# Kernel optimization log

Measured on AMD Instinct MI355X. Metric: run time of the kernel, lower is better.

The kernel has to match this reference:

```python
import math
import jax, jax.numpy as jnp
import numpy as np

B, S, D, H = 4, 2048, 1024, 16
HD = D // H
SAMPLING_FACTOR = 5.0


def setup_inputs() -> dict:
    key = jax.random.key(0)
    ks = jax.random.split(key, 6)
    std = 1.0 / math.sqrt(D)
    inp = {
        "x": jax.random.normal(ks[0], (B, S, D), dtype=jnp.float32),
        "Wq": jax.random.normal(ks[1], (D, D), dtype=jnp.float32) * std,
        "bq": jnp.zeros((D,), dtype=jnp.float32),
        "Wk": jax.random.normal(ks[2], (D, D), dtype=jnp.float32) * std,
        "bk": jnp.zeros((D,), dtype=jnp.float32),
        "Wv": jax.random.normal(ks[3], (D, D), dtype=jnp.float32) * std,
        "bv": jnp.zeros((D,), dtype=jnp.float32),
        "Wo": jax.random.normal(ks[4], (D, D), dtype=jnp.float32) * std,
        "bo": jnp.zeros((D,), dtype=jnp.float32),
        "sample_idx": jax.random.randint(ks[5], (S,), 0, S, dtype=jnp.int32),
    }
    return inp


def reference(x, Wq, bq, Wk, bk, Wv, bv, Wo, bo, sample_idx):
    batch, seq_len, d_model = x.shape
    scale = math.sqrt(HD)
    # u = number of top (active) queries; U_part = seq_len here (sampling saturates)
    u = max(1, min(seq_len, int(SAMPLING_FACTOR * math.log(seq_len + 1))))

    def proj(W, b):
        # [B,S,D] -> [B,H,S,hd]
        return (x @ W + b).reshape(batch, seq_len, H, HD).transpose(0, 2, 1, 3)

    Q = proj(Wq, bq)
    K = proj(Wk, bk)
    V = proj(Wv, bv)

    # sparsity measure over sampled keys (with replacement)
    K_sample = K[:, :, sample_idx, :]                     # [B,H,U,hd]
    scores_sample = jnp.einsum("bhsd,bhud->bhsu", Q, K_sample) / scale
    M = scores_sample.max(axis=-1) - scores_sample.mean(axis=-1)  # [B,H,S]

    _, top_idx = jax.lax.top_k(M, u)                      # [B,H,u]

    Q_reduce = jnp.take_along_axis(Q, top_idx[..., None], axis=2)  # [B,H,u,hd]
    attn_scores = jnp.einsum("bhud,bhsd->bhus", Q_reduce, K) / scale
    attn_probs = jax.nn.softmax(attn_scores, axis=-1)
    context = jnp.einsum("bhus,bhsd->bhud", attn_probs, V)        # [B,H,u,hd]

    # fill lazy queries with mean of V, scatter active-query contexts
    V_mean = V.mean(axis=2, keepdims=True)                # [B,H,1,hd]
    out = jnp.broadcast_to(V_mean, (batch, H, seq_len, HD))
    b_idx = jnp.arange(batch)[:, None, None]
    h_idx = jnp.arange(H)[None, :, None]
    out = out.at[b_idx, h_idx, top_idx].set(context)      # [B,H,S,hd]

    out = out.transpose(0, 2, 1, 3).reshape(batch, seq_len, d_model)
    return out @ Wo + bo
```

## Files before the change

### kernel.cpp

```cpp
#include <hip/hip_runtime.h>
#include <math.h>
#include <stdint.h>
#include <stddef.h>

#define BB 4
#define SS 2048
#define DD 1024
#define HH 16
#define HD 64
#define UU 38
#define BH (BB*HH)
#define NROWS (BB*SS)
#define QSZ (BB*HH*SS*HD)
#define NSPLIT 16
#define SPLEN (SS/NSPLIT)
#define QPAD 40

typedef unsigned short ushortT;
typedef unsigned int u32;
typedef __attribute__((ext_vector_type(8))) short bf16x8;
typedef __attribute__((ext_vector_type(4))) float f32x4;

static __device__ __forceinline__ ushortT f2bf(float f) {
  union { float f; unsigned int u; } v; v.f = f;
  unsigned int r = v.u + 0x7fffu + ((v.u >> 16) & 1u);
  return (ushortT)(r >> 16);
}
static __device__ __forceinline__ float bf2f(ushortT h) {
  union { unsigned int u; float f; } v; v.u = ((unsigned int)h) << 16; return v.f;
}
static __device__ __forceinline__ void gld16(const void* g, void* l) {
  __builtin_amdgcn_global_load_lds((const __attribute__((address_space(1))) u32*)g,
                                   (__attribute__((address_space(3))) u32*)l, 16, 0, 0);
}

__global__ __launch_bounds__(256) void split_x(
    const float* __restrict__ x, ushortT* __restrict__ xh, ushortT* __restrict__ xl)
{
  size_t i = ((size_t)blockIdx.x * 256 + threadIdx.x) * 8;
  float4 v0 = *(const float4*)&x[i];
  float4 v1 = *(const float4*)&x[i + 4];
  float fv[8] = {v0.x, v0.y, v0.z, v0.w, v1.x, v1.y, v1.z, v1.w};
  bf16x8 hv, lv;
#pragma unroll
  for (int j = 0; j < 8; ++j) {
    ushortT h = f2bf(fv[j]);
    hv[j] = (short)h;
    lv[j] = (short)f2bf(fv[j] - bf2f(h));
  }
  *(bf16x8*)&xh[i] = hv;
  *(bf16x8*)&xl[i] = lv;
}

__global__ __launch_bounds__(256) void splitT_kernel(
    const float* __restrict__ Wq, const float* __restrict__ Wk, const float* __restrict__ Wv,
    ushortT* __restrict__ WqhT, ushortT* __restrict__ WqlT,
    ushortT* __restrict__ WkhT, ushortT* __restrict__ WklT,
    ushortT* __restrict__ WvhT, ushortT* __restrict__ WvlT)
{
  __shared__ float tile[64][65];
  const int z = blockIdx.z;
  const float* W = (z == 0) ? Wq : (z == 1) ? Wk : Wv;
  ushortT* WhT = (z == 0) ? WqhT : (z == 1) ? WkhT : WvhT;
  ushortT* WlT = (z == 0) ? WqlT : (z == 1) ? WklT : WvlT;
  const int t = threadIdx.x;
  const int bk = blockIdx.y * 64, bn = blockIdx.x * 64;
  const int rr = t >> 4, c4 = (t & 15) * 4;
#pragma unroll
  for (int p = 0; p < 4; ++p) {
    int row = rr + p * 16;
    float4 v = *(const float4*)&W[(size_t)(bk + row) * DD + bn + c4];
    tile[row][c4] = v.x; tile[row][c4+1] = v.y; tile[row][c4+2] = v.z; tile[row][c4+3] = v.w;
  }
  __syncthreads();
  const int n = t & 63, ks = (t >> 6) * 16;
  union { ushortT us[16]; uint4 q[2]; } hb, lb;
#pragma unroll
  for (int j = 0; j < 16; ++j) {
    float f = tile[ks + j][n];
    ushortT h = f2bf(f);
    hb.us[j] = h;
    lb.us[j] = f2bf(f - bf2f(h));
  }
  size_t o = ((size_t)(bn + n) * DD + (size_t)(bk + ks)) >> 3;
  ((uint4*)WhT)[o] = hb.q[0]; ((uint4*)WhT)[o + 1] = hb.q[1];
  ((uint4*)WlT)[o] = lb.q[0]; ((uint4*)WlT)[o + 1] = lb.q[1];
}

__global__ __launch_bounds__(256) void dedupe_kernel(
    const int* __restrict__ sidx, int* __restrict__ uidx, int* __restrict__ ucount)
{
  __shared__ unsigned bm[64];
  __shared__ int base[64];
  const int t = threadIdx.x;
  if (t < 64) bm[t] = 0;
  __syncthreads();
  for (int s = t; s < SS; s += 256) {
    int v = sidx[s];
    atomicOr(&bm[v >> 5], 1u << (v & 31));
  }
  __syncthreads();
  if (t < 64) {
    int c = __popc(bm[t]);
    int pre = c;
#pragma unroll
    for (int off = 1; off < 64; off <<= 1) {
      int o = __shfl_up(pre, off, 64);
      if (t >= off) pre += o;
    }
    base[t] = pre - c;
    if (t == 63) ucount[0] = pre;
  }
  __syncthreads();
  if (t < 64) {
    unsigned m = bm[t];
    int o = base[t];
    while (m) {
      int b = __ffs(m) - 1;
      uidx[o++] = t * 32 + b;
      m &= m - 1;
    }
  }
  __syncthreads();
  int total = ucount[0];
  int padded = (total + 127) & ~127;
  int first = uidx[0];
  for (int i = total + t; i < padded; i += 256) uidx[i] = first;
}

__global__ __launch_bounds__(256, 4) void gemm_qkv(
    const ushortT* __restrict__ Axh, const ushortT* __restrict__ Axl,
    const ushortT* __restrict__ WqhT, const ushortT* __restrict__ WqlT,
    const ushortT* __restrict__ WkhT, const ushortT* __restrict__ WklT,
    const ushortT* __restrict__ WvhT, const ushortT* __restrict__ WvlT,
    const float* __restrict__ bq, const float* __restrict__ bk, const float* __restrict__ bv,
    ushortT* __restrict__ Qhg, ushortT* __restrict__ Qlg,
    ushortT* __restrict__ Khg, ushortT* __restrict__ Klg,
    float* __restrict__ V)
{
  __shared__ ushortT As[128 * 64];
  __shared__ ushortT Bs[128 * 64];
  const int t = threadIdx.x;
  const int lin = blockIdx.x;
  const int xcd = lin & 7;
  const int idx = lin >> 3;
  const int m_loc = idx & 7;
  const int n_idx = idx >> 3;
  const int m0 = (xcd * 8 + m_loc) * 128;
  const int p = n_idx >> 3;
  const int n0 = (n_idx & 7) * 128;
  const ushortT* Bh = (p == 0) ? WqhT : (p == 1) ? WkhT : WvhT;
  const ushortT* Bl = (p == 0) ? WqlT : (p == 1) ? WklT : WvlT;
  const float* bias = (p == 0) ? bq : (p == 1) ? bk : bv;
  const int NTk = (p == 2) ? 32 : 48;
  const int lane = t & 63, w = t >> 6;
  const int wr = w >> 1, wc = w & 1;
  const int fr = lane & 15, fs = lane >> 4;
  const int srow = t >> 3, sslot = t & 7;
  f32x4 acc[4][4];
#pragma unroll
  for (int i = 0; i < 4; ++i)
#pragma unroll
    for (int j = 0; j < 4; ++j) acc[i][j] = (f32x4){0.f, 0.f, 0.f, 0.f};

  for (int kt = 0; kt < NTk; ++kt) {
    const int seg = kt >> 4;
    const int rk0 = (kt & 15) * 64;
    const ushortT* a_src = (seg == 1) ? Axl : Axh;
    const ushortT* b_src = (seg == 2) ? Bl : Bh;
    __syncthreads();
#pragma unroll
    for (int is = 0; is < 4; ++is) {
      int row = is * 32 + srow;
      int soff = ((sslot ^ (row & 7)) * 8);
      int cb = (is * 256 + (t & 192)) * 8;
      gld16(&a_src[(size_t)(m0 + row) * DD + rk0 + soff], &As[cb]);
      gld16(&b_src[(size_t)(n0 + row) * DD + rk0 + soff], &Bs[cb]);
    }
    __syncthreads();
#pragma unroll
    for (int kk = 0; kk < 2; ++kk) {
      bf16x8 af[4], bf[4];
#pragma unroll
      for (int i = 0; i < 4; ++i) {
        int row = wr * 64 + i * 16 + fr;
        af[i] = *(const bf16x8*)&As[row * 64 + (((kk * 4 + fs) ^ (row & 7)) * 8)];
      }
#pragma unroll
      for (int j = 0; j < 4; ++j) {
        int row = wc * 64 + j * 16 + fr;
        bf[j] = *(const bf16x8*)&Bs[row * 64 + (((kk * 4 + fs) ^ (row & 7)) * 8)];
      }
#pragma unroll
      for (int i = 0; i < 4; ++i)
#pragma unroll
        for (int j = 0; j < 4; ++j)
          acc[i][j] = __builtin_amdgcn_mfma_f32_16x16x32_bf16(af[i], bf[j], acc[i][j], 0, 0, 0);
    }
  }
#pragma unroll
  for (int i = 0; i < 4; ++i) {
#pragma unroll
    for (int j = 0; j < 4; ++j) {
      int c = n0 + wc * 64 + j * 16 + fr;
      float bs = bias[c];
      int h = c >> 6, hd = c & 63;
#pragma unroll
      for (int r = 0; r < 4; ++r) {
        int m = m0 + wr * 64 + i * 16 + fs * 4 + r;
        int b = m >> 11, s = m & (SS - 1);
        size_t oidx = (((size_t)(b * HH + h)) * SS + s) * HD + hd;
        float val = acc[i][j][r] + bs;
        if (p == 2) {
          V[oidx] = val;
        } else {
          ushortT hv = f2bf(val);
          ushortT lv = f2bf(val - bf2f(hv));
          if (p == 0) { Qhg[oidx] = hv; Qlg[oidx] = lv; }
          else        { Khg[oidx] = hv; Klg[oidx] = lv; }
        }
      }
    }
  }
}

__global__ __launch_bounds__(256) void means_kernel(
    const ushortT* __restrict__ Khg, const ushortT* __restrict__ Klg,
    const float* __restrict__ V, const int* __restrict__ sidx,
    float* __restrict__ Kmean, float* __restrict__ Vmean)
{
  __shared__ float rk[4][64], rv[4][64];
  const int bh = blockIdx.x;
  const int t = threadIdx.x;
  const int d = t & 63, p = t >> 6;
  const float* Vb = V + (size_t)bh * SS * HD;
  float ka = 0.f, va = 0.f;
  for (int r = p * 512; r < (p + 1) * 512; ++r) {
    size_t ki = ((size_t)bh * SS + sidx[r]) * HD + d;
    ka += bf2f(Khg[ki]) + bf2f(Klg[ki]);
    va += Vb[(size_t)r * HD + d];
  }
  rk[p][d] = ka; rv[p][d] = va;
  __syncthreads();
  if (t < 64) {
    Kmean[bh * HD + t] = (rk[0][t] + rk[1][t] + rk[2][t] + rk[3][t]) * (1.0f / SS);
    Vmean[bh * HD + t] = (rv[0][t] + rv[1][t] + rv[2][t] + rv[3][t]) * (1.0f / SS);
  }
}

__global__ __launch_bounds__(256, 3) void m_mfma(
    const ushortT* __restrict__ Qhg, const ushortT* __restrict__ Qlg,
    const ushortT* __restrict__ Khg, const ushortT* __restrict__ Klg,
    const int* __restrict__ uidx, const int* __restrict__ ucount,
    const float* __restrict__ Kmean, float* __restrict__ M)
{
  __shared__ ushortT KhL[128 * 64], KlL[128 * 64];
  __shared__ float Mred[2][128];
  __shared__ float km[64];
  const int t = threadIdx.x;
  const int lin = blockIdx.x;
  const int swz = (lin & 7) * 128 + (lin >> 3);
  const int bh = swz >> 4;
  const int s0 = (swz & 15) * 128;
  const int lane = t & 63, w = t >> 6;
  const int wr = w >> 1, wc = w & 1;
  const int fr = lane & 15, fs = lane >> 4;
  if (t < 64) km[t] = Kmean[bh * HD + t];
  const int srow = t >> 3, sslot = t & 7;
  const int ntiles = (ucount[0] + 127) >> 7;
  const size_t qbase = (size_t)bh * SS + s0;
  float runmax[4][4];
#pragma unroll
  for (int i = 0; i < 4; ++i)
#pragma unroll
    for (int r = 0; r < 4; ++r) runmax[i][r] = -INFINITY;

  for (int ui = 0; ui < ntiles; ++ui) {
    __syncthreads();
#pragma unroll
    for (int is = 0; is < 4; ++is) {
      int row = is * 32 + srow;
      int gr = uidx[ui * 128 + row];
      int soff = ((sslot ^ (row & 7)) * 8);
      int cb = (is * 256 + (t & 192)) * 8;
      size_t ga = ((size_t)bh * SS + gr) * HD + soff;
      gld16(&Khg[ga], &KhL[cb]);
      gld16(&Klg[ga], &KlL[cb]);
    }
    __syncthreads();
    f32x4 acc[4][4];
#pragma unroll
    for (int i = 0; i < 4; ++i)
#pragma unroll
      for (int j = 0; j < 4; ++j) acc[i][j] = (f32x4){0.f, 0.f, 0.f, 0.f};
#pragma unroll
    for (int kk = 0; kk < 2; ++kk) {
      bf16x8 ah[4], al[4], bh[4], bl[4];
#pragma unroll
      for (int i = 0; i < 4; ++i) {
        size_t ga = (qbase + (size_t)(wr * 64 + i * 16 + fr)) * HD + kk * 32 + fs * 8;
        ah[i] = *(const bf16x8*)&Qhg[ga];
        al[i] = *(const bf16x8*)&Qlg[ga];
      }
#pragma unroll
      for (int j = 0; j < 4; ++j) {
        int row = wc * 64 + j * 16 + fr;
        int off = row * 64 + (((kk * 4 + fs) ^ (row & 7)) * 8);
        bh[j] = *(const bf16x8*)&KhL[off];
        bl[j] = *(const bf16x8*)&KlL[off];
      }
#pragma unroll
      for (int i = 0; i < 4; ++i)
#pragma unroll
        for (int j = 0; j < 4; ++j) {
          acc[i][j] = __builtin_amdgcn_mfma_f32_16x16x32_bf16(ah[i], bh[j], acc[i][j], 0, 0, 0);
          acc[i][j] = __builtin_amdgcn_mfma_f32_16x16x32_bf16(ah[i], bl[j], acc[i][j], 0, 0, 0);
          acc[i][j] = __builtin_amdgcn_mfma_f32_16x16x32_bf16(al[i], bh[j], acc[i][j], 0, 0, 0);
        }
    }
#pragma unroll
    for (int i = 0; i < 4; ++i)
#pragma unroll
      for (int j = 0; j < 4; ++j)
#pragma unroll
        for (int r = 0; r < 4; ++r) runmax[i][r] = fmaxf(runmax[i][r], acc[i][j][r]);
  }
#pragma unroll
  for (int i = 0; i < 4; ++i)
#pragma unroll
    for (int r = 0; r < 4; ++r) {
      float v = runmax[i][r];
      v = fmaxf(v, __shfl_xor(v, 1, 64));
      v = fmaxf(v, __shfl_xor(v, 2, 64));
      v = fmaxf(v, __shfl_xor(v, 4, 64));
      v = fmaxf(v, __shfl_xor(v, 8, 64));
      runmax[i][r] = v;
    }
  if (fr == 0) {
#pragma unroll
    for (int i = 0; i < 4; ++i)
#pragma unroll
      for (int r = 0; r < 4; ++r)
        Mred[wc][wr * 64 + i * 16 + fs * 4 + r] = runmax[i][r];
  }
  __syncthreads();
  if (t < 128) {
    float mx = fmaxf(Mred[0][t], Mred[1][t]);
    float md = 0.f;
    const ushortT* qh = &Qhg[(qbase + t) * HD];
    const ushortT* ql = &Qlg[(qbase + t) * HD];
#pragma unroll
    for (int k8 = 0; k8 < 8; ++k8) {
      bf16x8 hv = *(const bf16x8*)&qh[k8 * 8];
      bf16x8 lv = *(const bf16x8*)&ql[k8 * 8];
#pragma unroll
      for (int j = 0; j < 8; ++j)
        md += (bf2f((ushortT)hv[j]) + bf2f((ushortT)lv[j])) * km[k8 * 8 + j];
    }
    M[(size_t)bh * SS + s0 + t] = (mx - md) * 0.125f;
  }
}

__global__ __launch_bounds__(256) void topk_kernel(const float* __restrict__ M,
                                                   int* __restrict__ topi)
{
  __shared__ float rw[4];
  __shared__ int   ri4[4];
  __shared__ int   winner;
  const int t = threadIdx.x, bh = blockIdx.x;
  const int lane = t & 63, w = t >> 6;
  float v[8];
#pragma unroll
  for (int j = 0; j < 8; ++j) v[j] = M[(size_t)bh * SS + t + j * 256];
  for (int it = 0; it < UU; ++it) {
    float bv = v[0]; int bj = 0;
#pragma unroll
    for (int j = 1; j < 8; ++j) if (v[j] > bv) { bv = v[j]; bj = j; }
    int bs = t + bj * 256;
#pragma unroll
    for (int off = 32; off > 0; off >>= 1) {
      float ov = __shfl_xor(bv, off, 64);
      int os = __shfl_xor(bs, off, 64);
      if (ov > bv || (ov == bv && os < bs)) { bv = ov; bs = os; }
    }
    if (lane == 0) { rw[w] = bv; ri4[w] = bs; }
    __syncthreads();
    if (t == 0) {
      float fv = rw[0]; int fsx = ri4[0];
#pragma unroll
      for (int g = 1; g < 4; ++g)
        if (rw[g] > fv || (rw[g] == fv && ri4[g] < fsx)) { fv = rw[g]; fsx = ri4[g]; }
      topi[bh * UU + it] = fsx;
      winner = fsx;
    }
    __syncthreads();
    int wi = winner;
    if ((wi & 255) == t) {
      int jj = wi >> 8;
#pragma unroll
      for (int j = 0; j < 8; ++j) if (j == jj) v[j] = -INFINITY;
    }
  }
}

__global__ __launch_bounds__(256) void attn_flash(
    const ushortT* __restrict__ Qhg, const ushortT* __restrict__ Qlg,
    const ushortT* __restrict__ Khg, const ushortT* __restrict__ Klg,
    const float* __restrict__ V, const int* __restrict__ topi,
    float* __restrict__ pacc, float* __restrict__ pm, float* __restrict__ pl)
{
  __shared__ float Qt[64][68];
  __shared__ float KV[64][68];
  __shared__ float Ps[64][68];
  __shared__ float redA[16][64];
  __shared__ float redB[16][64];
  __shared__ float mrow[64], lrow[64], scl[64];
  const int t  = threadIdx.x;
  const int bh = blockIdx.x;
  const int sp = blockIdx.y;
  const float* Vb = V + (size_t)bh * SS * HD;
  if (t < 64) { mrow[t] = -INFINITY; lrow[t] = 0.f; }
  {
    int q = t >> 2, k4 = (t & 3) * 16;
    float fv[16];
#pragma unroll
    for (int e = 0; e < 16; ++e) fv[e] = 0.f;
    if (q < UU) {
      int qidx = topi[bh * UU + q];
      size_t ga = ((size_t)bh * SS + qidx) * HD + k4;
      bf16x8 h0 = *(const bf16x8*)&Qhg[ga];
      bf16x8 h1 = *(const bf16x8*)&Qhg[ga + 8];
      bf16x8 l0 = *(const bf16x8*)&Qlg[ga];
      bf16x8 l1 = *(const bf16x8*)&Qlg[ga + 8];
#pragma unroll
      for (int j = 0; j < 8; ++j) {
        fv[j]     = bf2f((ushortT)h0[j]) + bf2f((ushortT)l0[j]);
        fv[8 + j] = bf2f((ushortT)h1[j]) + bf2f((ushortT)l1[j]);
      }
    }
#pragma unroll
    for (int e = 0; e < 16; ++e) Qt[k4 + e][q] = fv[e];
  }
  const int q4 = (t & 15) * 4, j4g = (t >> 4) * 4, d4 = (t >> 4) * 4;
  const int lj = t >> 2, lk4 = (t & 3) * 16;
  float acc[4][4] = {};
  for (int s0 = sp * SPLEN; s0 < (sp + 1) * SPLEN; s0 += 64) {
    __syncthreads();
    {
      size_t ga = ((size_t)bh * SS + s0 + lj) * HD + lk4;
      bf16x8 h0 = *(const bf16x8*)&Khg[ga];
      bf16x8 h1 = *(const bf16x8*)&Khg[ga + 8];
      bf16x8 l0 = *(const bf16x8*)&Klg[ga];
      bf16x8 l1 = *(const bf16x8*)&Klg[ga + 8];
#pragma unroll
      for (int j = 0; j < 8; ++j) {
        KV[lk4 + j][lj]     = bf2f((ushortT)h0[j]) + bf2f((ushortT)l0[j]);
        KV[lk4 + 8 + j][lj] = bf2f((ushortT)h1[j]) + bf2f((ushortT)l1[j]);
      }
    }
    __syncthreads();
    float sacc[4][4] = {};
#pragma unroll 16
    for (int k = 0; k < 64; ++k) {
      float4 a = *(const float4*)&Qt[k][q4];
      float4 b = *(const float4*)&KV[k][j4g];
      sacc[0][0] += a.x*b.x; sacc[0][1] += a.x*b.y; sacc[0][2] += a.x*b.z; sacc[0][3] += a.x*b.w;
      sacc[1][0] += a.y*b.x; sacc[1][1] += a.y*b.y; sacc[1][2] += a.y*b.z; sacc[1][3] += a.y*b.w;
      sacc[2][0] += a.z*b.x; sacc[2][1] += a.z*b.y; sacc[2][2] += a.z*b.z; sacc[2][3] += a.z*b.w;
      sacc[3][0] += a.w*b.x; sacc[3][1] += a.w*b.y; sacc[3][2] += a.w*b.z; sacc[3][3] += a.w*b.w;
    }
#pragma unroll
    for (int i = 0; i < 4; ++i) {
      float mx = fmaxf(fmaxf(sacc[i][0], sacc[i][1]), fmaxf(sacc[i][2], sacc[i][3]));
      redA[t >> 4][q4 + i] = mx;
    }
    __syncthreads();
    if (t < 64) {
      float mx = redA[0][t];
#pragma unroll
      for (int g = 1; g < 16; ++g) mx = fmaxf(mx, redA[g][t]);
      float mn = fmaxf(mrow[t], mx * 0.125f);
      scl[t] = __expf(mrow[t] - mn);
      mrow[t] = mn;
    }
    __syncthreads();
    float4 vld[4];
#pragma unroll
    for (int i = 0; i < 4; ++i)
      vld[i] = *(const float4*)&Vb[(size_t)(s0 + lj) * HD + lk4 + 4 * i];
    float psum[4] = {};
#pragma unroll
    for (int i = 0; i < 4; ++i) {
#pragma unroll
      for (int j = 0; j < 4; ++j) {
        float e = __expf(sacc[i][j] * 0.125f - mrow[q4 + i]);
        Ps[j4g + j][q4 + i] = e;
        psum[i] += e;
      }
      redB[t >> 4][q4 + i] = psum[i];
    }
#pragma unroll
    for (int i = 0; i < 4; ++i)
      *(float4*)&KV[lj][lk4 + 4 * i] = vld[i];
    __syncthreads();
    if (t < 64) {
      float ts = redB[0][t];
#pragma unroll
      for (int g = 1; g < 16; ++g) ts += redB[g][t];
      lrow[t] = lrow[t] * scl[t] + ts;
    }
#pragma unroll
    for (int i = 0; i < 4; ++i) {
      float fsc = scl[q4 + i];
      acc[i][0] *= fsc; acc[i][1] *= fsc; acc[i][2] *= fsc; acc[i][3] *= fsc;
    }
#pragma unroll 16
    for (int j = 0; j < 64; ++j) {
      float4 a = *(const float4*)&Ps[j][q4];
      float4 b = *(const float4*)&KV[j][d4];
      acc[0][0] += a.x*b.x; acc[0][1] += a.x*b.y; acc[0][2] += a.x*b.z; acc[0][3] += a.x*b.w;
      acc[1][0] += a.y*b.x; acc[1][1] += a.y*b.y; acc[1][2] += a.y*b.z; acc[1][3] += a.y*b.w;
      acc[2][0] += a.z*b.x; acc[2][1] += a.z*b.y; acc[2][2] += a.z*b.z; acc[2][3] += a.z*b.w;
      acc[3][0] += a.w*b.x; acc[3][1] += a.w*b.y; acc[3][2] += a.w*b.z; acc[3][3] += a.w*b.w;
    }
  }
  const size_t pb = ((size_t)bh * NSPLIT + sp) * QPAD;
#pragma unroll
  for (int i = 0; i < 4; ++i) {
    int q = q4 + i;
    if (q < UU) {
#pragma unroll
      for (int j = 0; j < 4; ++j)
        pacc[(pb + q) * HD + d4 + j] = acc[i][j];
    }
  }
  if (t < UU) { pm[pb + t] = mrow[t]; pl[pb + t] = lrow[t]; }
}

__global__ __launch_bounds__(256) void attn_combine(
    const float* __restrict__ pacc, const float* __restrict__ pm,
    const float* __restrict__ pl, float* __restrict__ ctx)
{
  const int t  = threadIdx.x;
  const int bh = blockIdx.x;
  const int d = t & 63, qg = t >> 6;
  for (int q = qg; q < UU; q += 4) {
    float mv[NSPLIT];
    float ms = -INFINITY;
#pragma unroll
    for (int sp = 0; sp < NSPLIT; ++sp) {
      mv[sp] = pm[((size_t)bh * NSPLIT + sp) * QPAD + q];
      ms = fmaxf(ms, mv[sp]);
    }
    float l = 0.f, c = 0.f;
#pragma unroll
    for (int sp = 0; sp < NSPLIT; ++sp) {
      float wv = __expf(mv[sp] - ms);
      l += wv * pl[((size_t)bh * NSPLIT + sp) * QPAD + q];
      c += wv * pacc[(((size_t)bh * NSPLIT + sp) * QPAD + q) * HD + d];
    }
    ctx[((size_t)bh * UU + q) * HD + d] = c / l;
  }
}

__global__ __launch_bounds__(256) void base_kernel(
    const float* __restrict__ Vmean, const float* __restrict__ Wo,
    const float* __restrict__ bo, float* __restrict__ base)
{
  __shared__ float red[16][BB][16];
  const int t = threadIdx.x;
  const int cl = t & 15, kg = t >> 4;
  const int c = blockIdx.x * 16 + cl;
  float acc[BB] = {};
  for (int k = kg * 64; k < kg * 64 + 64; ++k) {
    float w = Wo[(size_t)k * DD + c];
#pragma unroll
    for (int b = 0; b < BB; ++b) acc[b] += Vmean[b * DD + k] * w;
  }
#pragma unroll
  for (int b = 0; b < BB; ++b) red[kg][b][cl] = acc[b];
  __syncthreads();
  if (t < 64) {
    int b = t >> 4, cc = blockIdx.x * 16 + (t & 15);
    float s = 0.f;
#pragma unroll
    for (int g = 0; g < 16; ++g) s += red[g][b][t & 15];
    base[b * DD + cc] = s + bo[cc];
  }
}

__global__ void fill_kernel(const float* __restrict__ base, float* __restrict__ out)
{
  size_t i = (size_t)blockIdx.x * 256 + threadIdx.x;
  float4 bv = ((const float4*)base)[(i >> 19) * 256 + (i & 255)];
  ((float4*)out)[i] = bv;
}

__global__ __launch_bounds__(256) void scatter_kernel(
    const float* __restrict__ ctx, const float* __restrict__ Vmean,
    const int* __restrict__ topi, const float* __restrict__ Wo,
    float* __restrict__ out)
{
  __shared__ float delta[64];
  const int t  = threadIdx.x;
  const int bh = blockIdx.x;
  const int u  = blockIdx.y;
  const int b = bh >> 4, h = bh & 15;
  const int s = topi[bh * UU + u];
  if (t < 64) delta[t] = ctx[((size_t)bh * UU + u) * HD + t] - Vmean[bh * HD + t];
  __syncthreads();
  float* orow = out + ((size_t)b * SS + s) * DD;
#pragma unroll
  for (int j = 0; j < 4; ++j) {
    int c = t + j * 256;
    float acc = 0.f;
#pragma unroll 8
    for (int d = 0; d < 64; ++d) acc += delta[d] * Wo[(size_t)(h * HD + d) * DD + c];
    atomicAdd(&orow[c], acc);
  }
}

extern "C" void kernel_launch(void* const* d_in, const int* in_sizes, int n_in,
                              void* d_out, int out_size, void* d_ws, size_t ws_size,
                              hipStream_t stream) {
  const float* x  = (const float*)d_in[0];
  const float* Wq = (const float*)d_in[1];
  const float* bq = (const float*)d_in[2];
  const float* Wk = (const float*)d_in[3];
  const float* bk = (const float*)d_in[4];
  const float* Wv = (const float*)d_in[5];
  const float* bv = (const float*)d_in[6];
  const float* Wo = (const float*)d_in[7];
  const float* bo = (const float*)d_in[8];
  const int* sidx = (const int*)d_in[9];
  float* out = (float*)d_out;

  float* f     = (float*)d_ws;
  float* V     = f;
  float* Kmean = f + (size_t)QSZ;
  float* Vmean = Kmean + BH * HD;
  float* Mbuf  = Vmean + BH * HD;
  float* base  = Mbuf + (size_t)BH * SS;
  float* ctx   = base + BB * DD;
  float* pacc  = ctx + (size_t)BH * UU * HD;
  float* pm    = pacc + (size_t)BH * NSPLIT * QPAD * HD;
  float* pl    = pm + (size_t)BH * NSPLIT * QPAD;
  int*   topi  = (int*)(pl + (size_t)BH * NSPLIT * QPAD);
  int*   uidx  = topi + 4096;
  int*   ucount= uidx + 4096;
  ushortT* usp = (ushortT*)(ucount + 64);
  ushortT* WqhT = usp;
  ushortT* WqlT = WqhT + (size_t)DD * DD;
  ushortT* WkhT = WqlT + (size_t)DD * DD;
  ushortT* WklT = WkhT + (size_t)DD * DD;
  ushortT* WvhT = WklT + (size_t)DD * DD;
  ushortT* WvlT = WvhT + (size_t)DD * DD;
  ushortT* xh   = WvlT + (size_t)DD * DD;
  ushortT* xl   = xh + (size_t)NROWS * DD;
  ushortT* Qhg  = xl + (size_t)NROWS * DD;
  ushortT* Qlg  = Qhg + (size_t)QSZ;
  ushortT* Khg  = Qlg + (size_t)QSZ;
  ushortT* Klg  = Khg + (size_t)QSZ;

  split_x<<<NROWS * DD / (256 * 8), 256, 0, stream>>>(x, xh, xl);
  splitT_kernel<<<dim3(16, 16, 3), 256, 0, stream>>>(Wq, Wk, Wv, WqhT, WqlT,
                                                     WkhT, WklT, WvhT, WvlT);
  dedupe_kernel<<<1, 256, 0, stream>>>(sidx, uidx, ucount);
  gemm_qkv<<<1536, 256, 0, stream>>>(xh, xl, WqhT, WqlT, WkhT, WklT, WvhT, WvlT,
                                     bq, bk, bv, Qhg, Qlg, Khg, Klg, V);
  means_kernel<<<BH, 256, 0, stream>>>(Khg, Klg, V, sidx, Kmean, Vmean);
  m_mfma<<<1024, 256, 0, stream>>>(Qhg, Qlg, Khg, Klg, uidx, ucount, Kmean, Mbuf);
  topk_kernel<<<BH, 256, 0, stream>>>(Mbuf, topi);
  attn_flash<<<dim3(BH, NSPLIT), 256, 0, stream>>>(Qhg, Qlg, Khg, Klg, V, topi, pacc, pm, pl);
  attn_combine<<<BH, 256, 0, stream>>>(pacc, pm, pl, ctx);
  base_kernel<<<DD / 16, 256, 0, stream>>>(Vmean, Wo, bo, base);
  fill_kernel<<<(NROWS * DD / 4) / 256, 256, 0, stream>>>(base, out);
  scatter_kernel<<<dim3(BH, UU), 256, 0, stream>>>(ctx, Vmean, topi, Wo, out);
}
```

Measured before the change: 421.0 us.

## Fuse V column sums into QKV GEMM epilogue and merge split-combine into scatter

The V mean is now accumulated in the QKV GEMM epilogue through a shared-memory reduction and atomicAdd into Vsum, which removes a full re-read of V in means_kernel. means_kernel now only computes the sampled-K sum and is split over 4 blocks per head with atomics, giving it more parallelism. The separate attn_combine kernel is removed and its split-softmax merge is done inside scatter_kernel, saving one launch and the ctx round trip. The costs are float atomics, which make the summation order nondeterministic, an extra barrier in the GEMM epilogue, and zeroing of the accumulators in dedupe_kernel.

```diff
diff --git a/kernel.cpp b/kernel.cpp
--- a/kernel.cpp
+++ b/kernel.cpp
@@ -88,11 +88,13 @@
 }
 
 __global__ __launch_bounds__(256) void dedupe_kernel(
-    const int* __restrict__ sidx, int* __restrict__ uidx, int* __restrict__ ucount)
+    const int* __restrict__ sidx, int* __restrict__ uidx, int* __restrict__ ucount,
+    float* __restrict__ Vsum, float* __restrict__ Ksum)
 {
   __shared__ unsigned bm[64];
   __shared__ int base[64];
   const int t = threadIdx.x;
+  for (int i = t; i < BH * HD; i += 256) { Vsum[i] = 0.f; Ksum[i] = 0.f; }
   if (t < 64) bm[t] = 0;
   __syncthreads();
   for (int s = t; s < SS; s += 256) {
@@ -136,7 +138,7 @@
     const float* __restrict__ bq, const float* __restrict__ bk, const float* __restrict__ bv,
     ushortT* __restrict__ Qhg, ushortT* __restrict__ Qlg,
     ushortT* __restrict__ Khg, ushortT* __restrict__ Klg,
-    float* __restrict__ V)
+    float* __restrict__ V, float* __restrict__ Vsum)
 {
   __shared__ ushortT As[128 * 64];
   __shared__ ushortT Bs[128 * 64];
@@ -198,6 +200,7 @@
           acc[i][j] = __builtin_amdgcn_mfma_f32_16x16x32_bf16(af[i], bf[j], acc[i][j], 0, 0, 0);
     }
   }
+  float csum[4] = {0.f, 0.f, 0.f, 0.f};
 #pragma unroll
   for (int i = 0; i < 4; ++i) {
 #pragma unroll
@@ -213,6 +216,7 @@
         float val = acc[i][j][r] + bs;
         if (p == 2) {
           V[oidx] = val;
+          csum[j] += val;
         } else {
           ushortT hv = f2bf(val);
           ushortT lv = f2bf(val - bf2f(hv));
@@ -222,37 +226,51 @@
       }
     }
   }
+  if (p == 2) {
+    __syncthreads();
+    float* red = (float*)As;
+    int slot = wr * 4 + fs;
+#pragma unroll
+    for (int j = 0; j < 4; ++j)
+      red[(wc * 64 + j * 16 + fr) * 8 + slot] = csum[j];
+    __syncthreads();
+    if (t < 128) {
+      float s = 0.f;
+#pragma unroll
+      for (int g = 0; g < 8; ++g) s += red[t * 8 + g];
+      int c = n0 + t;
+      int h = c >> 6, hd = c & 63;
+      atomicAdd(&Vsum[((m0 >> 11) * HH + h) * HD + hd], s);
+    }
+  }
 }
 
 __global__ __launch_bounds__(256) void means_kernel(
     const ushortT* __restrict__ Khg, const ushortT* __restrict__ Klg,
-    const float* __restrict__ V, const int* __restrict__ sidx,
-    float* __restrict__ Kmean, float* __restrict__ Vmean)
-{
-  __shared__ float rk[4][64], rv[4][64];
+    const int* __restrict__ sidx, float* __restrict__ Ksum)
+{
+  __shared__ float rk[4][64];
   const int bh = blockIdx.x;
+  const int sp = blockIdx.y;
   const int t = threadIdx.x;
-  const int d = t & 63, p = t >> 6;
-  const float* Vb = V + (size_t)bh * SS * HD;
-  float ka = 0.f, va = 0.f;
-  for (int r = p * 512; r < (p + 1) * 512; ++r) {
+  const int d = t & 63, pq = t >> 6;
+  float ka = 0.f;
+  const int r0 = sp * 512 + pq * 128;
+  for (int r = r0; r < r0 + 128; ++r) {
     size_t ki = ((size_t)bh * SS + sidx[r]) * HD + d;
     ka += bf2f(Khg[ki]) + bf2f(Klg[ki]);
-    va += Vb[(size_t)r * HD + d];
-  }
-  rk[p][d] = ka; rv[p][d] = va;
-  __syncthreads();
-  if (t < 64) {
-    Kmean[bh * HD + t] = (rk[0][t] + rk[1][t] + rk[2][t] + rk[3][t]) * (1.0f / SS);
-    Vmean[bh * HD + t] = (rv[0][t] + rv[1][t] + rv[2][t] + rv[3][t]) * (1.0f / SS);
-  }
+  }
+  rk[pq][d] = ka;
+  __syncthreads();
+  if (t < 64)
+    atomicAdd(&Ksum[bh * HD + t], rk[0][t] + rk[1][t] + rk[2][t] + rk[3][t]);
 }
 
 __global__ __launch_bounds__(256, 3) void m_mfma(
     const ushortT* __restrict__ Qhg, const ushortT* __restrict__ Qlg,
     const ushortT* __restrict__ Khg, const ushortT* __restrict__ Klg,
     const int* __restrict__ uidx, const int* __restrict__ ucount,
-    const float* __restrict__ Kmean, float* __restrict__ M)
+    const float* __restrict__ Ksum, float* __restrict__ M)
 {
   __shared__ ushortT KhL[128 * 64], KlL[128 * 64];
   __shared__ float Mred[2][128];
@@ -265,7 +283,7 @@
   const int lane = t & 63, w = t >> 6;
   const int wr = w >> 1, wc = w & 1;
   const int fr = lane & 15, fs = lane >> 4;
-  if (t < 64) km[t] = Kmean[bh * HD + t];
+  if (t < 64) km[t] = Ksum[bh * HD + t] * (1.0f / SS);
   const int srow = t >> 3, sslot = t & 7;
   const int ntiles = (ucount[0] + 127) >> 7;
   const size_t qbase = (size_t)bh * SS + s0;
@@ -537,34 +555,8 @@
   if (t < UU) { pm[pb + t] = mrow[t]; pl[pb + t] = lrow[t]; }
 }
 
-__global__ __launch_bounds__(256) void attn_combine(
-    const float* __restrict__ pacc, const float* __restrict__ pm,
-    const float* __restrict__ pl, float* __restrict__ ctx)
-{
-  const int t  = threadIdx.x;
-  const int bh = blockIdx.x;
-  const int d = t & 63, qg = t >> 6;
-  for (int q = qg; q < UU; q += 4) {
-    float mv[NSPLIT];
-    float ms = -INFINITY;
-#pragma unroll
-    for (int sp = 0; sp < NSPLIT; ++sp) {
-      mv[sp] = pm[((size_t)bh * NSPLIT + sp) * QPAD + q];
-      ms = fmaxf(ms, mv[sp]);
-    }
-    float l = 0.f, c = 0.f;
-#pragma unroll
-    for (int sp = 0; sp < NSPLIT; ++sp) {
-      float wv = __expf(mv[sp] - ms);
-      l += wv * pl[((size_t)bh * NSPLIT + sp) * QPAD + q];
-      c += wv * pacc[(((size_t)bh * NSPLIT + sp) * QPAD + q) * HD + d];
-    }
-    ctx[((size_t)bh * UU + q) * HD + d] = c / l;
-  }
-}
-
 __global__ __launch_bounds__(256) void base_kernel(
-    const float* __restrict__ Vmean, const float* __restrict__ Wo,
+    const float* __restrict__ Vsum, const float* __restrict__ Wo,
     const float* __restrict__ bo, float* __restrict__ base)
 {
   __shared__ float red[16][BB][16];
@@ -575,7 +567,7 @@
   for (int k = kg * 64; k < kg * 64 + 64; ++k) {
     float w = Wo[(size_t)k * DD + c];
 #pragma unroll
-    for (int b = 0; b < BB; ++b) acc[b] += Vmean[b * DD + k] * w;
+    for (int b = 0; b < BB; ++b) acc[b] += Vsum[b * DD + k] * w;
   }
 #pragma unroll
   for (int b = 0; b < BB; ++b) red[kg][b][cl] = acc[b];
@@ -585,7 +577,7 @@
     float s = 0.f;
 #pragma unroll
     for (int g = 0; g < 16; ++g) s += red[g][b][t & 15];
-    base[b * DD + cc] = s + bo[cc];
+    base[b * DD + cc] = s * (1.0f / SS) + bo[cc];
   }
 }
 
@@ -597,7 +589,8 @@
 }
 
 __global__ __launch_bounds__(256) void scatter_kernel(
-    const float* __restrict__ ctx, const float* __restrict__ Vmean,
+    const float* __restrict__ pacc, const float* __restrict__ pm,
+    const float* __restrict__ pl, const float* __restrict__ Vsum,
     const int* __restrict__ topi, const float* __restrict__ Wo,
     float* __restrict__ out)
 {
@@ -607,7 +600,23 @@
   const int u  = blockIdx.y;
   const int b = bh >> 4, h = bh & 15;
   const int s = topi[bh * UU + u];
-  if (t < 64) delta[t] = ctx[((size_t)bh * UU + u) * HD + t] - Vmean[bh * HD + t];
+  if (t < 64) {
+    float mv[NSPLIT];
+    float ms = -INFINITY;
+#pragma unroll
+    for (int sp = 0; sp < NSPLIT; ++sp) {
+      mv[sp] = pm[((size_t)bh * NSPLIT + sp) * QPAD + u];
+      ms = fmaxf(ms, mv[sp]);
+    }
+    float l = 0.f, c = 0.f;
+#pragma unroll
+    for (int sp = 0; sp < NSPLIT; ++sp) {
+      float wv = __expf(mv[sp] - ms);
+      l += wv * pl[((size_t)bh * NSPLIT + sp) * QPAD + u];
+      c += wv * pacc[(((size_t)bh * NSPLIT + sp) * QPAD + u) * HD + t];
+    }
+    delta[t] = c / l - Vsum[bh * HD + t] * (1.0f / SS);
+  }
   __syncthreads();
   float* orow = out + ((size_t)b * SS + s) * DD;
 #pragma unroll
@@ -637,9 +646,9 @@
 
   float* f     = (float*)d_ws;
   float* V     = f;
-  float* Kmean = f + (size_t)QSZ;
-  float* Vmean = Kmean + BH * HD;
-  float* Mbuf  = Vmean + BH * HD;
+  float* Ksum  = f + (size_t)QSZ;
+  float* Vsum  = Ksum + BH * HD;
+  float* Mbuf  = Vsum + BH * HD;
   float* base  = Mbuf + (size_t)BH * SS;
   float* ctx   = base + BB * DD;
   float* pacc  = ctx + (size_t)BH * UU * HD;
@@ -665,15 +674,14 @@
   split_x<<<NROWS * DD / (256 * 8), 256, 0, stream>>>(x, xh, xl);
   splitT_kernel<<<dim3(16, 16, 3), 256, 0, stream>>>(Wq, Wk, Wv, WqhT, WqlT,
                                                      WkhT, WklT, WvhT, WvlT);
-  dedupe_kernel<<<1, 256, 0, stream>>>(sidx, uidx, ucount);
+  dedupe_kernel<<<1, 256, 0, stream>>>(sidx, uidx, ucount, Vsum, Ksum);
   gemm_qkv<<<1536, 256, 0, stream>>>(xh, xl, WqhT, WqlT, WkhT, WklT, WvhT, WvlT,
-                                     bq, bk, bv, Qhg, Qlg, Khg, Klg, V);
-  means_kernel<<<BH, 256, 0, stream>>>(Khg, Klg, V, sidx, Kmean, Vmean);
-  m_mfma<<<1024, 256, 0, stream>>>(Qhg, Qlg, Khg, Klg, uidx, ucount, Kmean, Mbuf);
+                                     bq, bk, bv, Qhg, Qlg, Khg, Klg, V, Vsum);
+  means_kernel<<<dim3(BH, 4), 256, 0, stream>>>(Khg, Klg, sidx, Ksum);
+  m_mfma<<<1024, 256, 0, stream>>>(Qhg, Qlg, Khg, Klg, uidx, ucount, Ksum, Mbuf);
   topk_kernel<<<BH, 256, 0, stream>>>(Mbuf, topi);
   attn_flash<<<dim3(BH, NSPLIT), 256, 0, stream>>>(Qhg, Qlg, Khg, Klg, V, topi, pacc, pm, pl);
-  attn_combine<<<BH, 256, 0, stream>>>(pacc, pm, pl, ctx);
-  base_kernel<<<DD / 16, 256, 0, stream>>>(Vmean, Wo, bo, base);
+  base_kernel<<<DD / 16, 256, 0, stream>>>(Vsum, Wo, bo, base);
   fill_kernel<<<(NROWS * DD / 4) / 256, 256, 0, stream>>>(base, out);
-  scatter_kernel<<<dim3(BH, UU), 256, 0, stream>>>(ctx, Vmean, topi, Wo, out);
-}
+  scatter_kernel<<<dim3(BH, UU), 256, 0, stream>>>(pacc, pm, pl, Vsum, topi, Wo, out);
+}
```

Result: faster. 388.3 us, median of 2 (-7.8%).
